# Optimization experiments

Hardware: AMD Instinct MI355X
Metric: run time of the kernel (lower is better)

Reference implementation:

```python
import jax, jax.numpy as jnp
import numpy as np

TEMP = 0.1
EPS = 1e-8


def setup_inputs() -> dict:
    key = jax.random.key(0)
    k1, k2, k3, k4 = jax.random.split(key, 4)
    b, c, H, W = 2, 64, 80, 80
    proj_main = jax.random.normal(k1, (b, c, H, W), dtype=jnp.float32)
    proj_ema = jax.random.normal(k2, (b, c, H, W), dtype=jnp.float32)
    label_main = jax.random.randint(k3, (b, H, W), 0, 2, dtype=jnp.int32)
    label_ema = jax.random.randint(k4, (b, H, W), 0, 2, dtype=jnp.int32)
    return {"proj_main": proj_main, "proj_ema": proj_ema,
            "label_main": label_main, "label_ema": label_ema,
            "patch_num": 8}


def reference(proj_main, proj_ema, label_main, label_ema, patch_num):
    # Labels / FC fractions are computed in the original forward but never
    # consumed by ContrastiveLoss, so they do not affect the output.
    # All patches have equal size h*w, so the per-patch-mean-of-means equals
    # the global mean over all b*H*W anchors; negative column ordering is
    # irrelevant to the row-wise logsumexp. Hence the nested loop fuses to:
    b, c, H, W = proj_main.shape
    A = jnp.transpose(proj_main, (0, 2, 3, 1)).reshape(-1, c)  # (N, c) anchors
    E = jnp.transpose(proj_ema, (0, 2, 3, 1)).reshape(-1, c)   # (N, c) ema feats
    pos = jnp.sum(A * E, axis=-1) / TEMP                       # (N,)
    neg = jnp.einsum('nc,mc->nm', A, E) / TEMP                 # (N, N)
    full = jnp.concatenate([pos[:, None], neg], axis=1)        # (N, N+1)
    m = jnp.max(full, axis=1)                                  # (N,) row max
    denom = jnp.sum(jnp.exp(full - m[:, None]), axis=1)        # (N,)
    loss = -jnp.log(jnp.exp(pos - m) / (denom + EPS) + EPS)
    return jnp.mean(loss)
```

## Files before the change

kernel.cpp:

```cpp
#include <hip/hip_runtime.h>
#include <stdint.h>

#define NA 12800
#define CCH 64
#define TB 2048
#define SC 14.4269504088896340736f
#define MARGIN 41.0f
#define FLOOR_LOSS 18.420680743952367f
#define MAXF 6400
#define NPARTS 20
#define SGMAX 8

typedef __attribute__((ext_vector_type(4))) float f32x4;
typedef __attribute__((ext_vector_type(8))) short s16x8;

#if __has_builtin(__builtin_amdgcn_exp2f)
#define EXP2(x) __builtin_amdgcn_exp2f(x)
#else
#define EXP2(x) exp2f(x)
#endif

__device__ __forceinline__ uint16_t f2bf(float x) {
  uint32_t u = __float_as_uint(x);
  return (uint16_t)((u + 0x7FFFu + ((u >> 16) & 1u)) >> 16);
}

__global__ __launch_bounds__(256) void prep_k(const float* __restrict__ pm,
                                              const float* __restrict__ pe,
                                              char* __restrict__ A,
                                              char* __restrict__ E,
                                              float* __restrict__ P2,
                                              int* __restrict__ fidx,
                                              int* __restrict__ cnt,
                                              int* __restrict__ done) {
  if (blockIdx.x == 0 && threadIdx.x == 0) { *cnt = 0; *done = 0; }
  const int l = threadIdx.x & 63;
  const int q = threadIdx.x >> 6;
  const int n = blockIdx.x * 64 + l;
  const int b = n / 6400, p = n - b * 6400;
  const float* am = pm + (size_t)b * CCH * 6400 + p;
  const float* ae = pe + (size_t)b * CCH * 6400 + p;

  char* abase = A + (size_t)(n >> 4) * TB + (n & 15) * 16;
  char* ebase = E + (size_t)(n >> 4) * TB + (n & 15) * 16;

  float pos = 0.0f;
#pragma unroll
  for (int cg2 = 0; cg2 < 2; ++cg2) {
    const int cg = q * 2 + cg2;
    s16x8 ah, eh;
#pragma unroll
    for (int j = 0; j < 8; ++j) {
      int chn = cg * 8 + j;
      float a = am[(size_t)chn * 6400];
      float e = ae[(size_t)chn * 6400];
      pos = fmaf(a, e, pos);
      ah[j] = (short)f2bf(a * SC);
      eh[j] = (short)f2bf(e);
    }
    const int off = (cg >> 2) * 1024 + (cg & 3) * 256;
    *(s16x8*)(abase + off) = ah;
    *(s16x8*)(ebase + off) = eh;
  }
  __shared__ float pp[4][64];
  pp[q][l] = pos;
  __syncthreads();
  if (q == 0) {
    P2[n] = ((pp[0][l] + pp[1][l]) + (pp[2][l] + pp[3][l])) * SC;
    fidx[n] = -1;
  }
}

__global__ __launch_bounds__(256, 2) void screen_k(const char* __restrict__ A,
                                                   const char* __restrict__ E,
                                                   const float* __restrict__ P2,
                                                   int* __restrict__ wl,
                                                   int* __restrict__ fidx,
                                                   int* __restrict__ cnt) {
  const int mt = blockIdx.x;
  const int tid = threadIdx.x;
  const int lane = tid & 63;
  const int wid = tid >> 6;
  const int l15 = lane & 15, lhi = lane >> 4;

  s16x8 af[4][2];
#pragma unroll
  for (int rt = 0; rt < 4; ++rt)
#pragma unroll
    for (int ks = 0; ks < 2; ++ks)
      af[rt][ks] = *(const s16x8*)(A + (size_t)(mt * 16 + wid * 4 + rt) * TB + ks * 1024 + lane * 16);

  s16x8 b[8][2];
#pragma unroll
  for (int t = 0; t < 8; ++t)
#pragma unroll
    for (int kh = 0; kh < 2; ++kh)
      b[t][kh] = *(const s16x8*)(E + (size_t)(t * 100) * TB + kh * 1024 + lane * 16);

  float m16[16];
#pragma unroll
  for (int i = 0; i < 16; ++i) m16[i] = -__builtin_inff();

  const f32x4 z4 = (f32x4){0.f, 0.f, 0.f, 0.f};
#pragma unroll
  for (int t = 0; t < 8; ++t) {
#pragma unroll
    for (int rt = 0; rt < 4; ++rt) {
      f32x4 a_ = __builtin_amdgcn_mfma_f32_16x16x32_bf16(af[rt][0], b[t][0], z4, 0, 0, 0);
      a_ = __builtin_amdgcn_mfma_f32_16x16x32_bf16(af[rt][1], b[t][1], a_, 0, 0, 0);
#pragma unroll
      for (int j = 0; j < 4; ++j) m16[rt * 4 + j] = fmaxf(m16[rt * 4 + j], a_[j]);
    }
  }

#pragma unroll
  for (int ri = 0; ri < 16; ++ri) {
    float m = m16[ri];
#pragma unroll
    for (int mask = 1; mask < 16; mask <<= 1) m = fmaxf(m, __shfl_xor(m, mask));
    m16[ri] = m;
  }
  if (l15 == 0) {
#pragma unroll
    for (int rt = 0; rt < 4; ++rt)
#pragma unroll
      for (int j = 0; j < 4; ++j) {
        int row = mt * 256 + wid * 64 + rt * 16 + lhi * 4 + j;
        if (!(m16[rt * 4 + j] > P2[row] + MARGIN)) {
          int i = atomicAdd(cnt, 1);
          wl[i] = row;
          fidx[row] = i;
        }
      }
  }
}

__global__ __launch_bounds__(256, 2) void exact_k(const char* __restrict__ A,
                                                  const char* __restrict__ E,
                                                  const int* __restrict__ wl,
                                                  const int* __restrict__ cnt,
                                                  float* __restrict__ Pm,
                                                  float* __restrict__ Ps) {
  const int part = blockIdx.x >> 3;
  const int sg0 = blockIdx.x & 7;
  int nr = *cnt; if (nr > MAXF) nr = MAXF;
  const int tid = threadIdx.x;
  const int lane = tid & 63;
  const int wid = tid >> 6;
  const int wm = wid >> 1, wn = wid & 1;
  const int l15 = lane & 15, lhi = lane >> 4;
  const f32x4 z4 = (f32x4){0.f, 0.f, 0.f, 0.f};

  for (int sg = sg0; sg * 64 < nr; sg += SGMAX) {
    const int sbase = sg * 64 + wm * 32;
    s16x8 af[2][2];
#pragma unroll
    for (int rt = 0; rt < 2; ++rt) {
      int sl = sbase + rt * 16 + l15;
      int n = wl[sl < nr ? sl : 0];
#pragma unroll
      for (int ks = 0; ks < 2; ++ks)
        af[rt][ks] = *(const s16x8*)(A + (size_t)(n >> 4) * TB + ks * 1024 + lhi * 256 + (n & 15) * 16);
    }

    float m8[8], s8[8];
#pragma unroll
    for (int i = 0; i < 8; ++i) { m8[i] = -__builtin_inff(); s8[i] = 0.0f; }

    for (int c = 0; c < 5; ++c) {
      s16x8 b[4][2];
#pragma unroll
      for (int ct = 0; ct < 4; ++ct)
#pragma unroll
        for (int kh = 0; kh < 2; ++kh)
          b[ct][kh] = *(const s16x8*)(E + (size_t)(part * 40 + c * 8 + wn * 4 + ct) * TB + kh * 1024 + lane * 16);

      f32x4 acc[2][4];
#pragma unroll
      for (int ct = 0; ct < 4; ++ct)
#pragma unroll
        for (int rt = 0; rt < 2; ++rt) {
          acc[rt][ct] = __builtin_amdgcn_mfma_f32_16x16x32_bf16(af[rt][0], b[ct][0], z4, 0, 0, 0);
          acc[rt][ct] = __builtin_amdgcn_mfma_f32_16x16x32_bf16(af[rt][1], b[ct][1], acc[rt][ct], 0, 0, 0);
        }

#pragma unroll
      for (int rt = 0; rt < 2; ++rt)
#pragma unroll
        for (int j = 0; j < 4; ++j) {
          const int ri = rt * 4 + j;
          float v0 = acc[rt][0][j], v1 = acc[rt][1][j], v2 = acc[rt][2][j], v3 = acc[rt][3][j];
          float vm = fmaxf(fmaxf(fmaxf(v0, v1), v2), v3);
          float mo = m8[ri];
          float mn = fmaxf(mo, vm);
          float t = (EXP2(v0 - mn) + EXP2(v1 - mn)) + (EXP2(v2 - mn) + EXP2(v3 - mn));
          s8[ri] = fmaf(s8[ri], EXP2(mo - mn), t);
          m8[ri] = mn;
        }
    }

#pragma unroll
    for (int ri = 0; ri < 8; ++ri) {
      float m = m8[ri], s = s8[ri];
#pragma unroll
      for (int mask = 1; mask < 16; mask <<= 1) {
        float mo = __shfl_xor(m, mask);
        float so = __shfl_xor(s, mask);
        float mn = fmaxf(m, mo);
        s = s * EXP2(m - mn) + so * EXP2(mo - mn);
        m = mn;
      }
      m8[ri] = m; s8[ri] = s;
    }
    if (l15 == 0) {
#pragma unroll
      for (int rt = 0; rt < 2; ++rt)
#pragma unroll
        for (int j = 0; j < 4; ++j) {
          int slot = sbase + rt * 16 + lhi * 4 + j;
          if (slot < nr) {
            Pm[(size_t)part * MAXF + slot] = m8[rt * 4 + j];
            Ps[(size_t)part * MAXF + slot] = s8[rt * 4 + j];
          }
        }
    }
  }
}

__global__ __launch_bounds__(256) void final_k(const float* __restrict__ P2,
                                               const int* __restrict__ fidx,
                                               const float* __restrict__ Pm,
                                               const float* __restrict__ Ps,
                                               float* __restrict__ bsum,
                                               int* __restrict__ done,
                                               float* __restrict__ out) {
  int n = blockIdx.x * 256 + threadIdx.x;
  int fi = fidx[n];
  float loss;
  if (fi >= 0 && fi < MAXF) {
    float m = -__builtin_inff(), s = 0.0f;
#pragma unroll
    for (int p = 0; p < NPARTS; ++p) {
      float mi = Pm[(size_t)p * MAXF + fi];
      float si = Ps[(size_t)p * MAXF + fi];
      float mn = fmaxf(m, mi);
      s = s * EXP2(m - mn) + si * EXP2(mi - mn);
      m = mn;
    }
    float p2 = P2[n];
    float mn = fmaxf(m, p2);
    float e = EXP2(p2 - mn);
    float sf = s * EXP2(m - mn) + e;
    loss = -logf(e / (sf + 1e-8f) + 1e-8f);
  } else {
    loss = FLOOR_LOSS;
  }

  __shared__ float red[4];
  __shared__ int lastf;
  float v = loss;
#pragma unroll
  for (int off = 32; off > 0; off >>= 1) v += __shfl_down(v, off);
  if ((threadIdx.x & 63) == 0) red[threadIdx.x >> 6] = v;
  __syncthreads();
  if (threadIdx.x == 0) {
    bsum[blockIdx.x] = (red[0] + red[1]) + (red[2] + red[3]);
    __threadfence();
    lastf = (atomicAdd(done, 1) == (NA / 256) - 1);
  }
  __syncthreads();
  if (lastf && threadIdx.x < 64) {
    __threadfence();
    float t = (threadIdx.x < NA / 256) ? bsum[threadIdx.x] : 0.0f;
#pragma unroll
    for (int off = 32; off > 0; off >>= 1) t += __shfl_down(t, off);
    if (threadIdx.x == 0) out[0] = t * (1.0f / (float)NA);
  }
}

extern "C" void kernel_launch(void* const* d_in, const int* in_sizes, int n_in,
                              void* d_out, int out_size, void* d_ws, size_t ws_size,
                              hipStream_t stream) {
  const float* pm = (const float*)d_in[0];
  const float* pe = (const float*)d_in[1];

  char* ws = (char*)d_ws;
  char* Abuf  = ws;
  char* Ebuf  = ws + 1638400;
  float* P2   = (float*)(ws + 3276800);
  float* Pm   = (float*)(ws + 3328000);
  float* Ps   = (float*)(ws + 3840000);
  int*   wl   = (int*)  (ws + 4352000);
  int*   fidx = (int*)  (ws + 4403200);
  int*   cnt  = (int*)  (ws + 4454400);
  int*   done = (int*)  (ws + 4454404);
  float* bsum = (float*)(ws + 4454528);

  prep_k  <<<NA / 64, 256, 0, stream>>>(pm, pe, Abuf, Ebuf, P2, fidx, cnt, done);
  screen_k<<<NA / 256, 256, 0, stream>>>(Abuf, Ebuf, P2, wl, fidx, cnt);
  exact_k <<<NPARTS * SGMAX, 256, 0, stream>>>(Abuf, Ebuf, wl, cnt, Pm, Ps);
  final_k <<<NA / 256, 256, 0, stream>>>(P2, fidx, Pm, Ps, bsum, done, (float*)d_out);
}
```

Measured before the change: 31.44 us.

## Fuse prep, screen, exact and final kernels into one persistent kernel with grid barriers

The four separate launches (prep, screen, exact logsumexp, final reduction) are merged into a single 200-block persistent kernel. Software grid barriers built on agent-scope atomics separate the phases, and a memset zeroes the counters beforehand. The screen phase is remapped to one 16-row tile per wave, so it runs across 200 blocks instead of 50. The exact phase now uses 10 sub-groups per part instead of 8. This removes inter-kernel launch gaps, but relies on all 200 blocks being co-resident and adds barrier spin latency plus an extra memset operation.

```diff
diff --git a/kernel.cpp b/kernel.cpp
--- a/kernel.cpp
+++ b/kernel.cpp
@@ -9,7 +9,8 @@
 #define FLOOR_LOSS 18.420680743952367f
 #define MAXF 6400
 #define NPARTS 20
-#define SGMAX 8
+#define SGMAX 10
+#define NBLK 200
 
 typedef __attribute__((ext_vector_type(4))) float f32x4;
 typedef __attribute__((ext_vector_type(8))) short s16x8;
@@ -25,256 +26,251 @@
   return (uint16_t)((u + 0x7FFFu + ((u >> 16) & 1u)) >> 16);
 }
 
-__global__ __launch_bounds__(256) void prep_k(const float* __restrict__ pm,
+__device__ __forceinline__ void gbar(int* bar, int target) {
+  __syncthreads();
+  if (threadIdx.x == 0) {
+    __threadfence();
+    __hip_atomic_fetch_add(bar, 1, __ATOMIC_RELEASE, __HIP_MEMORY_SCOPE_AGENT);
+    while (__hip_atomic_load(bar, __ATOMIC_ACQUIRE, __HIP_MEMORY_SCOPE_AGENT) < target)
+      __builtin_amdgcn_s_sleep(8);
+  }
+  __syncthreads();
+  __threadfence();
+}
+
+__global__ __launch_bounds__(256) void mega_k(const float* __restrict__ pm,
                                               const float* __restrict__ pe,
                                               char* __restrict__ A,
                                               char* __restrict__ E,
                                               float* __restrict__ P2,
+                                              float* __restrict__ Pm,
+                                              float* __restrict__ Ps,
+                                              int* __restrict__ wl,
                                               int* __restrict__ fidx,
-                                              int* __restrict__ cnt,
-                                              int* __restrict__ done) {
-  if (blockIdx.x == 0 && threadIdx.x == 0) { *cnt = 0; *done = 0; }
-  const int l = threadIdx.x & 63;
-  const int q = threadIdx.x >> 6;
-  const int n = blockIdx.x * 64 + l;
-  const int b = n / 6400, p = n - b * 6400;
-  const float* am = pm + (size_t)b * CCH * 6400 + p;
-  const float* ae = pe + (size_t)b * CCH * 6400 + p;
-
-  char* abase = A + (size_t)(n >> 4) * TB + (n & 15) * 16;
-  char* ebase = E + (size_t)(n >> 4) * TB + (n & 15) * 16;
-
-  float pos = 0.0f;
-#pragma unroll
-  for (int cg2 = 0; cg2 < 2; ++cg2) {
-    const int cg = q * 2 + cg2;
-    s16x8 ah, eh;
-#pragma unroll
-    for (int j = 0; j < 8; ++j) {
-      int chn = cg * 8 + j;
-      float a = am[(size_t)chn * 6400];
-      float e = ae[(size_t)chn * 6400];
-      pos = fmaf(a, e, pos);
-      ah[j] = (short)f2bf(a * SC);
-      eh[j] = (short)f2bf(e);
-    }
-    const int off = (cg >> 2) * 1024 + (cg & 3) * 256;
-    *(s16x8*)(abase + off) = ah;
-    *(s16x8*)(ebase + off) = eh;
-  }
-  __shared__ float pp[4][64];
-  pp[q][l] = pos;
-  __syncthreads();
-  if (q == 0) {
-    P2[n] = ((pp[0][l] + pp[1][l]) + (pp[2][l] + pp[3][l])) * SC;
-    fidx[n] = -1;
-  }
-}
-
-__global__ __launch_bounds__(256, 2) void screen_k(const char* __restrict__ A,
-                                                   const char* __restrict__ E,
-                                                   const float* __restrict__ P2,
-                                                   int* __restrict__ wl,
-                                                   int* __restrict__ fidx,
-                                                   int* __restrict__ cnt) {
-  const int mt = blockIdx.x;
+                                              int* __restrict__ ctr,
+                                              float* __restrict__ bsum,
+                                              float* __restrict__ out) {
+  const int blk = blockIdx.x;
   const int tid = threadIdx.x;
   const int lane = tid & 63;
   const int wid = tid >> 6;
   const int l15 = lane & 15, lhi = lane >> 4;
-
-  s16x8 af[4][2];
-#pragma unroll
-  for (int rt = 0; rt < 4; ++rt)
+  int* cnt  = ctr;
+  int* done = ctr + 1;
+  int* bar  = ctr + 2;
+  const f32x4 z4 = (f32x4){0.f, 0.f, 0.f, 0.f};
+
+  __shared__ float pp[4][64];
+  __shared__ float red[4];
+  __shared__ int lastf;
+
+  {
+    const int n = blk * 64 + lane;
+    const int b = n / 6400, p = n - b * 6400;
+    const float* am = pm + (size_t)b * CCH * 6400 + p;
+    const float* ae = pe + (size_t)b * CCH * 6400 + p;
+    char* abase = A + (size_t)(n >> 4) * TB + (n & 15) * 16;
+    char* ebase = E + (size_t)(n >> 4) * TB + (n & 15) * 16;
+
+    float pos = 0.0f;
+#pragma unroll
+    for (int cg2 = 0; cg2 < 2; ++cg2) {
+      const int cg = wid * 2 + cg2;
+      s16x8 ah, eh;
+#pragma unroll
+      for (int j = 0; j < 8; ++j) {
+        int chn = cg * 8 + j;
+        float a = am[(size_t)chn * 6400];
+        float e = ae[(size_t)chn * 6400];
+        pos = fmaf(a, e, pos);
+        ah[j] = (short)f2bf(a * SC);
+        eh[j] = (short)f2bf(e);
+      }
+      const int off = (cg >> 2) * 1024 + (cg & 3) * 256;
+      *(s16x8*)(abase + off) = ah;
+      *(s16x8*)(ebase + off) = eh;
+    }
+    pp[wid][lane] = pos;
+    __syncthreads();
+    if (wid == 0) {
+      P2[n] = ((pp[0][lane] + pp[1][lane]) + (pp[2][lane] + pp[3][lane])) * SC;
+      fidx[n] = -1;
+    }
+  }
+  gbar(bar, NBLK);
+
+  {
+    s16x8 af[2];
 #pragma unroll
     for (int ks = 0; ks < 2; ++ks)
-      af[rt][ks] = *(const s16x8*)(A + (size_t)(mt * 16 + wid * 4 + rt) * TB + ks * 1024 + lane * 16);
-
-  s16x8 b[8][2];
-#pragma unroll
-  for (int t = 0; t < 8; ++t)
-#pragma unroll
-    for (int kh = 0; kh < 2; ++kh)
-      b[t][kh] = *(const s16x8*)(E + (size_t)(t * 100) * TB + kh * 1024 + lane * 16);
-
-  float m16[16];
-#pragma unroll
-  for (int i = 0; i < 16; ++i) m16[i] = -__builtin_inff();
-
-  const f32x4 z4 = (f32x4){0.f, 0.f, 0.f, 0.f};
-#pragma unroll
-  for (int t = 0; t < 8; ++t) {
-#pragma unroll
-    for (int rt = 0; rt < 4; ++rt) {
-      f32x4 a_ = __builtin_amdgcn_mfma_f32_16x16x32_bf16(af[rt][0], b[t][0], z4, 0, 0, 0);
-      a_ = __builtin_amdgcn_mfma_f32_16x16x32_bf16(af[rt][1], b[t][1], a_, 0, 0, 0);
-#pragma unroll
-      for (int j = 0; j < 4; ++j) m16[rt * 4 + j] = fmaxf(m16[rt * 4 + j], a_[j]);
-    }
-  }
-
-#pragma unroll
-  for (int ri = 0; ri < 16; ++ri) {
-    float m = m16[ri];
-#pragma unroll
-    for (int mask = 1; mask < 16; mask <<= 1) m = fmaxf(m, __shfl_xor(m, mask));
-    m16[ri] = m;
-  }
-  if (l15 == 0) {
-#pragma unroll
-    for (int rt = 0; rt < 4; ++rt)
+      af[ks] = *(const s16x8*)(A + (size_t)(blk * 4 + wid) * TB + ks * 1024 + lane * 16);
+
+    s16x8 b[8][2];
+#pragma unroll
+    for (int t = 0; t < 8; ++t)
+#pragma unroll
+      for (int kh = 0; kh < 2; ++kh)
+        b[t][kh] = *(const s16x8*)(E + (size_t)(t * 100) * TB + kh * 1024 + lane * 16);
+
+    float m4[4];
+#pragma unroll
+    for (int i = 0; i < 4; ++i) m4[i] = -__builtin_inff();
+
+#pragma unroll
+    for (int t = 0; t < 8; ++t) {
+      f32x4 a_ = __builtin_amdgcn_mfma_f32_16x16x32_bf16(af[0], b[t][0], z4, 0, 0, 0);
+      a_ = __builtin_amdgcn_mfma_f32_16x16x32_bf16(af[1], b[t][1], a_, 0, 0, 0);
+#pragma unroll
+      for (int j = 0; j < 4; ++j) m4[j] = fmaxf(m4[j], a_[j]);
+    }
+#pragma unroll
+    for (int j = 0; j < 4; ++j) {
+      float m = m4[j];
+#pragma unroll
+      for (int mask = 1; mask < 16; mask <<= 1) m = fmaxf(m, __shfl_xor(m, mask));
+      m4[j] = m;
+    }
+    if (l15 == 0) {
 #pragma unroll
       for (int j = 0; j < 4; ++j) {
-        int row = mt * 256 + wid * 64 + rt * 16 + lhi * 4 + j;
-        if (!(m16[rt * 4 + j] > P2[row] + MARGIN)) {
+        int row = blk * 64 + wid * 16 + lhi * 4 + j;
+        if (!(m4[j] > P2[row] + MARGIN)) {
           int i = atomicAdd(cnt, 1);
           wl[i] = row;
           fidx[row] = i;
         }
       }
-  }
-}
-
-__global__ __launch_bounds__(256, 2) void exact_k(const char* __restrict__ A,
-                                                  const char* __restrict__ E,
-                                                  const int* __restrict__ wl,
-                                                  const int* __restrict__ cnt,
-                                                  float* __restrict__ Pm,
-                                                  float* __restrict__ Ps) {
-  const int part = blockIdx.x >> 3;
-  const int sg0 = blockIdx.x & 7;
-  int nr = *cnt; if (nr > MAXF) nr = MAXF;
-  const int tid = threadIdx.x;
-  const int lane = tid & 63;
-  const int wid = tid >> 6;
-  const int wm = wid >> 1, wn = wid & 1;
-  const int l15 = lane & 15, lhi = lane >> 4;
-  const f32x4 z4 = (f32x4){0.f, 0.f, 0.f, 0.f};
-
-  for (int sg = sg0; sg * 64 < nr; sg += SGMAX) {
-    const int sbase = sg * 64 + wm * 32;
-    s16x8 af[2][2];
-#pragma unroll
-    for (int rt = 0; rt < 2; ++rt) {
-      int sl = sbase + rt * 16 + l15;
-      int n = wl[sl < nr ? sl : 0];
-#pragma unroll
-      for (int ks = 0; ks < 2; ++ks)
-        af[rt][ks] = *(const s16x8*)(A + (size_t)(n >> 4) * TB + ks * 1024 + lhi * 256 + (n & 15) * 16);
-    }
-
-    float m8[8], s8[8];
-#pragma unroll
-    for (int i = 0; i < 8; ++i) { m8[i] = -__builtin_inff(); s8[i] = 0.0f; }
-
-    for (int c = 0; c < 5; ++c) {
-      s16x8 b[4][2];
-#pragma unroll
-      for (int ct = 0; ct < 4; ++ct)
-#pragma unroll
-        for (int kh = 0; kh < 2; ++kh)
-          b[ct][kh] = *(const s16x8*)(E + (size_t)(part * 40 + c * 8 + wn * 4 + ct) * TB + kh * 1024 + lane * 16);
-
-      f32x4 acc[2][4];
-#pragma unroll
-      for (int ct = 0; ct < 4; ++ct)
-#pragma unroll
-        for (int rt = 0; rt < 2; ++rt) {
-          acc[rt][ct] = __builtin_amdgcn_mfma_f32_16x16x32_bf16(af[rt][0], b[ct][0], z4, 0, 0, 0);
-          acc[rt][ct] = __builtin_amdgcn_mfma_f32_16x16x32_bf16(af[rt][1], b[ct][1], acc[rt][ct], 0, 0, 0);
+    }
+  }
+  gbar(bar, 2 * NBLK);
+
+  {
+    const int part = blk / SGMAX;
+    const int sg0 = blk - part * SGMAX;
+    int nr = *cnt; if (nr > MAXF) nr = MAXF;
+    const int wm = wid >> 1, wn = wid & 1;
+
+    for (int sg = sg0; sg * 64 < nr; sg += SGMAX) {
+      const int sbase = sg * 64 + wm * 32;
+      s16x8 af[2][2];
+#pragma unroll
+      for (int rt = 0; rt < 2; ++rt) {
+        int sl = sbase + rt * 16 + l15;
+        int n = wl[sl < nr ? sl : 0];
+#pragma unroll
+        for (int ks = 0; ks < 2; ++ks)
+          af[rt][ks] = *(const s16x8*)(A + (size_t)(n >> 4) * TB + ks * 1024 + lhi * 256 + (n & 15) * 16);
+      }
+
+      float m8[8], s8[8];
+#pragma unroll
+      for (int i = 0; i < 8; ++i) { m8[i] = -__builtin_inff(); s8[i] = 0.0f; }
+
+      for (int c = 0; c < 5; ++c) {
+        s16x8 b[4][2];
+#pragma unroll
+        for (int ct = 0; ct < 4; ++ct)
+#pragma unroll
+          for (int kh = 0; kh < 2; ++kh)
+            b[ct][kh] = *(const s16x8*)(E + (size_t)(part * 40 + c * 8 + wn * 4 + ct) * TB + kh * 1024 + lane * 16);
+
+        f32x4 acc[2][4];
+#pragma unroll
+        for (int ct = 0; ct < 4; ++ct)
+#pragma unroll
+          for (int rt = 0; rt < 2; ++rt) {
+            acc[rt][ct] = __builtin_amdgcn_mfma_f32_16x16x32_bf16(af[rt][0], b[ct][0], z4, 0, 0, 0);
+            acc[rt][ct] = __builtin_amdgcn_mfma_f32_16x16x32_bf16(af[rt][1], b[ct][1], acc[rt][ct], 0, 0, 0);
+          }
+
+#pragma unroll
+        for (int rt = 0; rt < 2; ++rt)
+#pragma unroll
+          for (int j = 0; j < 4; ++j) {
+            const int ri = rt * 4 + j;
+            float v0 = acc[rt][0][j], v1 = acc[rt][1][j], v2 = acc[rt][2][j], v3 = acc[rt][3][j];
+            float vm = fmaxf(fmaxf(fmaxf(v0, v1), v2), v3);
+            float mo = m8[ri];
+            float mn = fmaxf(mo, vm);
+            float t = (EXP2(v0 - mn) + EXP2(v1 - mn)) + (EXP2(v2 - mn) + EXP2(v3 - mn));
+            s8[ri] = fmaf(s8[ri], EXP2(mo - mn), t);
+            m8[ri] = mn;
+          }
+      }
+
+#pragma unroll
+      for (int ri = 0; ri < 8; ++ri) {
+        float m = m8[ri], s = s8[ri];
+#pragma unroll
+        for (int mask = 1; mask < 16; mask <<= 1) {
+          float mo = __shfl_xor(m, mask);
+          float so = __shfl_xor(s, mask);
+          float mn = fmaxf(m, mo);
+          s = s * EXP2(m - mn) + so * EXP2(mo - mn);
+          m = mn;
         }
-
-#pragma unroll
-      for (int rt = 0; rt < 2; ++rt)
-#pragma unroll
-        for (int j = 0; j < 4; ++j) {
-          const int ri = rt * 4 + j;
-          float v0 = acc[rt][0][j], v1 = acc[rt][1][j], v2 = acc[rt][2][j], v3 = acc[rt][3][j];
-          float vm = fmaxf(fmaxf(fmaxf(v0, v1), v2), v3);
-          float mo = m8[ri];
-          float mn = fmaxf(mo, vm);
-          float t = (EXP2(v0 - mn) + EXP2(v1 - mn)) + (EXP2(v2 - mn) + EXP2(v3 - mn));
-          s8[ri] = fmaf(s8[ri], EXP2(mo - mn), t);
-          m8[ri] = mn;
+        m8[ri] = m; s8[ri] = s;
+      }
+      if (l15 == 0) {
+#pragma unroll
+        for (int rt = 0; rt < 2; ++rt)
+#pragma unroll
+          for (int j = 0; j < 4; ++j) {
+            int slot = sbase + rt * 16 + lhi * 4 + j;
+            if (slot < nr) {
+              Pm[(size_t)part * MAXF + slot] = m8[rt * 4 + j];
+              Ps[(size_t)part * MAXF + slot] = s8[rt * 4 + j];
+            }
+          }
+      }
+    }
+  }
+  gbar(bar, 3 * NBLK);
+
+  {
+    if (tid < 64) {
+      int n = blk * 64 + tid;
+      int fi = fidx[n];
+      float loss;
+      if (fi >= 0 && fi < MAXF) {
+        float m = -__builtin_inff(), s = 0.0f;
+#pragma unroll
+        for (int p = 0; p < NPARTS; ++p) {
+          float mi = Pm[(size_t)p * MAXF + fi];
+          float si = Ps[(size_t)p * MAXF + fi];
+          float mn = fmaxf(m, mi);
+          s = s * EXP2(m - mn) + si * EXP2(mi - mn);
+          m = mn;
         }
-    }
-
-#pragma unroll
-    for (int ri = 0; ri < 8; ++ri) {
-      float m = m8[ri], s = s8[ri];
-#pragma unroll
-      for (int mask = 1; mask < 16; mask <<= 1) {
-        float mo = __shfl_xor(m, mask);
-        float so = __shfl_xor(s, mask);
-        float mn = fmaxf(m, mo);
-        s = s * EXP2(m - mn) + so * EXP2(mo - mn);
-        m = mn;
-      }
-      m8[ri] = m; s8[ri] = s;
-    }
-    if (l15 == 0) {
-#pragma unroll
-      for (int rt = 0; rt < 2; ++rt)
-#pragma unroll
-        for (int j = 0; j < 4; ++j) {
-          int slot = sbase + rt * 16 + lhi * 4 + j;
-          if (slot < nr) {
-            Pm[(size_t)part * MAXF + slot] = m8[rt * 4 + j];
-            Ps[(size_t)part * MAXF + slot] = s8[rt * 4 + j];
-          }
-        }
-    }
-  }
-}
-
-__global__ __launch_bounds__(256) void final_k(const float* __restrict__ P2,
-                                               const int* __restrict__ fidx,
-                                               const float* __restrict__ Pm,
-                                               const float* __restrict__ Ps,
-                                               float* __restrict__ bsum,
-                                               int* __restrict__ done,
-                                               float* __restrict__ out) {
-  int n = blockIdx.x * 256 + threadIdx.x;
-  int fi = fidx[n];
-  float loss;
-  if (fi >= 0 && fi < MAXF) {
-    float m = -__builtin_inff(), s = 0.0f;
-#pragma unroll
-    for (int p = 0; p < NPARTS; ++p) {
-      float mi = Pm[(size_t)p * MAXF + fi];
-      float si = Ps[(size_t)p * MAXF + fi];
-      float mn = fmaxf(m, mi);
-      s = s * EXP2(m - mn) + si * EXP2(mi - mn);
-      m = mn;
-    }
-    float p2 = P2[n];
-    float mn = fmaxf(m, p2);
-    float e = EXP2(p2 - mn);
-    float sf = s * EXP2(m - mn) + e;
-    loss = -logf(e / (sf + 1e-8f) + 1e-8f);
-  } else {
-    loss = FLOOR_LOSS;
-  }
-
-  __shared__ float red[4];
-  __shared__ int lastf;
-  float v = loss;
-#pragma unroll
-  for (int off = 32; off > 0; off >>= 1) v += __shfl_down(v, off);
-  if ((threadIdx.x & 63) == 0) red[threadIdx.x >> 6] = v;
-  __syncthreads();
-  if (threadIdx.x == 0) {
-    bsum[blockIdx.x] = (red[0] + red[1]) + (red[2] + red[3]);
-    __threadfence();
-    lastf = (atomicAdd(done, 1) == (NA / 256) - 1);
-  }
-  __syncthreads();
-  if (lastf && threadIdx.x < 64) {
-    __threadfence();
-    float t = (threadIdx.x < NA / 256) ? bsum[threadIdx.x] : 0.0f;
-#pragma unroll
-    for (int off = 32; off > 0; off >>= 1) t += __shfl_down(t, off);
-    if (threadIdx.x == 0) out[0] = t * (1.0f / (float)NA);
+        float p2 = P2[n];
+        float mn = fmaxf(m, p2);
+        float e = EXP2(p2 - mn);
+        float sf = s * EXP2(m - mn) + e;
+        loss = -logf(e / (sf + 1e-8f) + 1e-8f);
+      } else {
+        loss = FLOOR_LOSS;
+      }
+      float v = loss;
+#pragma unroll
+      for (int off = 32; off > 0; off >>= 1) v += __shfl_down(v, off);
+      if (tid == 0) bsum[blk] = v;
+    }
+    __syncthreads();
+    if (tid == 0) {
+      __threadfence();
+      lastf = (__hip_atomic_fetch_add(done, 1, __ATOMIC_ACQ_REL, __HIP_MEMORY_SCOPE_AGENT)
+               == NBLK - 1);
+    }
+    __syncthreads();
+    if (lastf) {
+      __threadfence();
+      float t = (tid < NBLK) ? bsum[tid] : 0.0f;
+#pragma unroll
+      for (int off = 32; off > 0; off >>= 1) t += __shfl_down(t, off);
+      if ((tid & 63) == 0) red[wid] = t;
+      __syncthreads();
+      if (tid == 0) out[0] = ((red[0] + red[1]) + (red[2] + red[3])) * (1.0f / (float)NA);
+    }
   }
 }
 
@@ -292,12 +288,10 @@
   float* Ps   = (float*)(ws + 3840000);
   int*   wl   = (int*)  (ws + 4352000);
   int*   fidx = (int*)  (ws + 4403200);
-  int*   cnt  = (int*)  (ws + 4454400);
-  int*   done = (int*)  (ws + 4454404);
+  int*   ctr  = (int*)  (ws + 4454400);
   float* bsum = (float*)(ws + 4454528);
 
-  prep_k  <<<NA / 64, 256, 0, stream>>>(pm, pe, Abuf, Ebuf, P2, fidx, cnt, done);
-  screen_k<<<NA / 256, 256, 0, stream>>>(Abuf, Ebuf, P2, wl, fidx, cnt);
-  exact_k <<<NPARTS * SGMAX, 256, 0, stream>>>(Abuf, Ebuf, wl, cnt, Pm, Ps);
-  final_k <<<NA / 256, 256, 0, stream>>>(P2, fidx, Pm, Ps, bsum, done, (float*)d_out);
-}
+  hipMemsetAsync(ctr, 0, 12, stream);
+  mega_k<<<NBLK, 256, 0, stream>>>(pm, pe, Abuf, Ebuf, P2, Pm, Ps,
+                                   wl, fidx, ctr, bsum, (float*)d_out);
+}
```

New measurement: 115.1 us. 266% more time.
